# Optimization experiments

Measured on AMD Instinct MI355X. Metric: run time of the kernel, lower is better.

## Reference

```python
import jax, jax.numpy as jnp
import numpy as np

N, E, H, L, C = 65536, 524288, 256, 9, 4096
MAXID, IDD = 64, 8
INC = 3 + IDD  # geo(3) + id embedding(8)
HQ = H // 4


def setup_inputs() -> dict:
    key = jax.random.key(0)
    ks = jax.random.split(key, 18)
    s = lambda fan: 1.0 / np.sqrt(fan)
    d = {}
    d["x_geo"] = jax.random.normal(ks[0], (N, 3), jnp.float32)
    d["id_index"] = jax.random.randint(ks[1], (N,), 0, MAXID + 1)
    d["edge_index"] = jax.random.randint(ks[2], (2, E), 0, N)
    d["cluster"] = jax.random.randint(ks[3], (N,), 0, C)
    d["id_emb"] = jax.random.normal(ks[4], (MAXID + 1, IDD), jnp.float32) * 0.02
    d["enc_w1"] = jax.random.normal(ks[5], (INC, HQ), jnp.float32) * s(INC)
    d["enc_b1"] = jnp.zeros((HQ,), jnp.float32)
    d["enc_w2"] = jax.random.normal(ks[6], (HQ, HQ), jnp.float32) * s(HQ)
    d["enc_b2"] = jnp.zeros((HQ,), jnp.float32)
    d["enc_w3"] = jax.random.normal(ks[7], (HQ, H), jnp.float32) * s(HQ)
    d["enc_b3"] = jnp.zeros((H,), jnp.float32)
    d["skip_w"] = jax.random.normal(ks[8], (INC, H), jnp.float32) * s(INC)
    d["skip_b"] = jnp.zeros((H,), jnp.float32)
    d["gcn_w"] = jax.random.normal(ks[9], (L, H, H), jnp.float32) * s(H)
    d["gcn_b"] = jnp.zeros((L, H), jnp.float32)
    d["ln_g"] = jnp.ones((L, H), jnp.float32)
    d["ln_b"] = jnp.zeros((L, H), jnp.float32)
    return d


def _gelu(x):
    return jax.nn.gelu(x, approximate=False)  # torch GELU default is exact


def reference(x_geo, id_index, edge_index, cluster, id_emb,
              enc_w1, enc_b1, enc_w2, enc_b2, enc_w3, enc_b3,
              skip_w, skip_b, gcn_w, gcn_b, ln_g, ln_b):
    n = x_geo.shape[0]
    # node features: geo + id embedding
    node = jnp.concatenate([x_geo, id_emb[id_index]], axis=-1)  # [N, 11]
    # ResBottleneck encoder
    h = _gelu(node @ enc_w1 + enc_b1)
    h = _gelu(h @ enc_w2 + enc_b2)
    h = h @ enc_w3 + enc_b3
    x = _gelu(node @ skip_w + skip_b + h)  # [N, H]

    src, dst = edge_index[0], edge_index[1]
    e = src.shape[0]
    # degree with self-loops (GCN symmetric norm)
    deg = jax.ops.segment_sum(jnp.ones((e,), x.dtype), dst, num_segments=n) + 1.0
    dis = jax.lax.rsqrt(deg)  # deg^-1/2, [N]
    self_norm = (dis * dis)[:, None]
    edge_norm = (dis[src] * dis[dst])[:, None]

    orig = x
    for i in range(L):
        hi = x @ gcn_w[i]                                    # [N, H]
        msg = hi[src] * edge_norm                            # gather + scale
        agg = jax.ops.segment_sum(msg, dst, num_segments=n)  # scatter-add
        agg = agg + hi * self_norm + gcn_b[i]                # self-loop + bias
        # LayerNorm
        mu = agg.mean(-1, keepdims=True)
        var = ((agg - mu) ** 2).mean(-1, keepdims=True)
        xn = (agg - mu) * jax.lax.rsqrt(var + 1e-5) * ln_g[i] + ln_b[i]
        x = jax.nn.relu(xn)  # dropout p=1e-4 inactive in eval mode
        if i == 0:
            x = x + orig  # residual after first conv only

    # avg_pool_x: mean of node features per cluster
    cnt = jax.ops.segment_sum(jnp.ones((n,), x.dtype), cluster, num_segments=C)
    pooled = jax.ops.segment_sum(x, cluster, num_segments=C) / jnp.maximum(cnt, 1.0)[:, None]
    # F.normalize(p=2, dim=0, eps=1e-6): per-feature L2 norm across clusters
    nrm = jnp.sqrt(jnp.sum(pooled * pooled, axis=0, keepdims=True))
    return pooled / jnp.maximum(nrm, 1e-6)
```

## Files before the change

### kernel.cpp

```cpp
#include <hip/hip_runtime.h>
#include <math.h>

#define N_NODES 65536
#define N_EDGES 524288
#define HDIM 256
#define NLAYERS 9
#define NCLUST 4096
#define HQ 64
#define INCF 11

typedef __attribute__((ext_vector_type(8))) short short8v;
typedef __attribute__((ext_vector_type(4))) float f32x4;

__device__ __forceinline__ float gelu_exact(float v) {
    return 0.5f * v * (1.0f + erff(v * 0.70710678118654752440f));
}

__device__ __forceinline__ unsigned short f2bf(float f) {
    union { float f; unsigned u; } a; a.f = f;
    unsigned r = a.u + 0x7FFFu + ((a.u >> 16) & 1u);
    return (unsigned short)(r >> 16);
}

__device__ __forceinline__ float bf2f(unsigned short h) {
    union { unsigned u; float f; } a; a.u = ((unsigned)h) << 16;
    return a.f;
}

__device__ __forceinline__ void split_bf(float v, unsigned short& h, unsigned short& l) {
    h = f2bf(v);
    l = f2bf(v - bf2f(h));
}

__device__ __forceinline__ void gload16(const void* g, void* l) {
    __builtin_amdgcn_global_load_lds(
        (const __attribute__((address_space(1))) void*)g,
        (__attribute__((address_space(3))) void*)l,
        16, 0, 0);
}

__global__ __launch_bounds__(256) void encoder_kernel(
    const float* __restrict__ x_geo, const int* __restrict__ id_index,
    const float* __restrict__ id_emb,
    const float* __restrict__ w1, const float* __restrict__ b1,
    const float* __restrict__ w2, const float* __restrict__ b2,
    const float* __restrict__ w3, const float* __restrict__ b3,
    const float* __restrict__ sw, const float* __restrict__ sb,
    unsigned short* __restrict__ xh, unsigned short* __restrict__ xl)
{
    int wid = blockIdx.x * 4 + (threadIdx.x >> 6);
    int lane = threadIdx.x & 63;
    int nbase = wid * 4;
    if (nbase >= N_NODES) return;

    float nf[4][INCF];
#pragma unroll
    for (int j = 0; j < 4; ++j) {
        int node = nbase + j;
        nf[j][0] = x_geo[node * 3 + 0];
        nf[j][1] = x_geo[node * 3 + 1];
        nf[j][2] = x_geo[node * 3 + 2];
        int idv = id_index[node];
#pragma unroll
        for (int k = 0; k < 8; ++k) nf[j][3 + k] = id_emb[idv * 8 + k];
    }

    float h1[4];
    {
        float b = b1[lane];
        float a0 = b, a1 = b, a2 = b, a3 = b;
#pragma unroll
        for (int k = 0; k < INCF; ++k) {
            float wv = w1[k * HQ + lane];
            a0 += nf[0][k] * wv; a1 += nf[1][k] * wv;
            a2 += nf[2][k] * wv; a3 += nf[3][k] * wv;
        }
        h1[0] = gelu_exact(a0); h1[1] = gelu_exact(a1);
        h1[2] = gelu_exact(a2); h1[3] = gelu_exact(a3);
    }

    float h2[4];
    {
        float b = b2[lane];
        float a0 = b, a1 = b, a2 = b, a3 = b;
        for (int k = 0; k < HQ; ++k) {
            float wv = w2[k * HQ + lane];
            a0 += __shfl(h1[0], k) * wv; a1 += __shfl(h1[1], k) * wv;
            a2 += __shfl(h1[2], k) * wv; a3 += __shfl(h1[3], k) * wv;
        }
        h2[0] = gelu_exact(a0); h2[1] = gelu_exact(a1);
        h2[2] = gelu_exact(a2); h2[3] = gelu_exact(a3);
    }

    float a4[4][4];
#pragma unroll
    for (int j0 = 0; j0 < 4; ++j0) {
        float b = b3[j0 * 64 + lane] + sb[j0 * 64 + lane];
#pragma unroll
        for (int j = 0; j < 4; ++j) a4[j][j0] = b;
    }
    for (int k = 0; k < HQ; ++k) {
        float wv0 = w3[k * HDIM + 0 * 64 + lane];
        float wv1 = w3[k * HDIM + 1 * 64 + lane];
        float wv2 = w3[k * HDIM + 2 * 64 + lane];
        float wv3 = w3[k * HDIM + 3 * 64 + lane];
#pragma unroll
        for (int j = 0; j < 4; ++j) {
            float hk = __shfl(h2[j], k);
            a4[j][0] += hk * wv0; a4[j][1] += hk * wv1;
            a4[j][2] += hk * wv2; a4[j][3] += hk * wv3;
        }
    }
#pragma unroll
    for (int k = 0; k < INCF; ++k) {
        float wv0 = sw[k * HDIM + 0 * 64 + lane];
        float wv1 = sw[k * HDIM + 1 * 64 + lane];
        float wv2 = sw[k * HDIM + 2 * 64 + lane];
        float wv3 = sw[k * HDIM + 3 * 64 + lane];
#pragma unroll
        for (int j = 0; j < 4; ++j) {
            float nk = nf[j][k];
            a4[j][0] += nk * wv0; a4[j][1] += nk * wv1;
            a4[j][2] += nk * wv2; a4[j][3] += nk * wv3;
        }
    }
#pragma unroll
    for (int j = 0; j < 4; ++j) {
        int node = nbase + j;
#pragma unroll
        for (int j0 = 0; j0 < 4; ++j0) {
            float v = gelu_exact(a4[j][j0]);
            unsigned short h, l;
            split_bf(v, h, l);
            xh[(size_t)node * HDIM + j0 * 64 + lane] = h;
            xl[(size_t)node * HDIM + j0 * 64 + lane] = l;
        }
    }
}

__global__ void count_kernel(const int* __restrict__ dst, int* __restrict__ degi) {
    int e = blockIdx.x * blockDim.x + threadIdx.x;
    if (e < N_EDGES) atomicAdd(&degi[dst[e]], 1);
}

__global__ void dis_kernel(const int* __restrict__ degi, float* __restrict__ dis) {
    int n = blockIdx.x * blockDim.x + threadIdx.x;
    if (n < N_NODES) dis[n] = rsqrtf((float)degi[n] + 1.0f);
}

__global__ __launch_bounds__(1024) void scan_kernel(const int* __restrict__ degi,
                                                    int* __restrict__ off) {
    __shared__ int part[1024];
    int t = threadIdx.x;
    int base = t * 64;
    int s = 0;
    for (int j = 0; j < 64; ++j) s += degi[base + j];
    part[t] = s;
    __syncthreads();
    for (int d = 1; d < 1024; d <<= 1) {
        int v = (t >= d) ? part[t - d] : 0;
        __syncthreads();
        part[t] += v;
        __syncthreads();
    }
    int run = (t == 0) ? 0 : part[t - 1];
    for (int j = 0; j < 64; ++j) {
        off[base + j] = run;
        run += degi[base + j];
    }
    if (t == 1023) off[N_NODES] = run;
}

__global__ void fill_kernel(const int* __restrict__ src, const int* __restrict__ dst,
                            const int* __restrict__ off, int* __restrict__ cursor,
                            int* __restrict__ csr_src) {
    int e = blockIdx.x * blockDim.x + threadIdx.x;
    if (e >= N_EDGES) return;
    int d = dst[e];
    int pos = off[d] + atomicAdd(&cursor[d], 1);
    csr_src[pos] = src[e];
}

__global__ __launch_bounds__(256) void wtrans_kernel(const float* __restrict__ w,
                                                     unsigned short* __restrict__ wth,
                                                     unsigned short* __restrict__ wtl_) {
    __shared__ float t[32][257];
    int l = blockIdx.y, kb = blockIdx.x;
    const float* wl = w + (size_t)l * HDIM * HDIM + (size_t)kb * 32 * HDIM;
#pragma unroll
    for (int it = 0; it < 32; ++it) {
        int idx = it * 256 + threadIdx.x;
        t[idx >> 8][idx & 255] = wl[idx];
    }
    __syncthreads();
    unsigned short* wh = wth + (size_t)l * HDIM * HDIM + kb * 32;
    unsigned short* wl2 = wtl_ + (size_t)l * HDIM * HDIM + kb * 32;
    int k = threadIdx.x & 31, n0 = threadIdx.x >> 5;
#pragma unroll
    for (int it = 0; it < 32; ++it) {
        int n = it * 8 + n0;
        unsigned short h, lo;
        split_bf(t[k][n], h, lo);
        wh[(size_t)n * HDIM + k] = h;
        wl2[(size_t)n * HDIM + k] = lo;
    }
}

__global__ __launch_bounds__(512) void mfma_gemm_kernel(
    const unsigned short* __restrict__ Ah, const unsigned short* __restrict__ Al,
    const unsigned short* __restrict__ Bh, const unsigned short* __restrict__ Bl,
    float* __restrict__ C_)
{
    __shared__ unsigned short AsH[128 * 32];
    __shared__ unsigned short AsL[128 * 32];
    __shared__ unsigned short BsH[256 * 32];
    __shared__ unsigned short BsL[256 * 32];
    int tid = threadIdx.x;
    int w = tid >> 6, l = tid & 63;
    int bm = blockIdx.x;
    int wm = w >> 2, wn = w & 3;
    int fr = l & 15, fs = l >> 4;

    f32x4 acc[4][4];
#pragma unroll
    for (int m = 0; m < 4; ++m)
#pragma unroll
        for (int n = 0; n < 4; ++n) acc[m][n] = (f32x4){0.f, 0.f, 0.f, 0.f};

    const size_t aoff = (size_t)(bm * 128) * HDIM;
    const int rowA = tid >> 2, subA = tid & 3;
    const int sgA = subA ^ ((rowA >> 1) & 3);
    const int rowB1 = (512 + tid) >> 2;
    const int sgB1 = subA ^ ((rowB1 >> 1) & 3);

    unsigned short* lAH = &AsH[(w * 64) * 8];
    unsigned short* lAL = &AsL[(w * 64) * 8];
    unsigned short* lBH0 = &BsH[(w * 64) * 8];
    unsigned short* lBL0 = &BsL[(w * 64) * 8];
    unsigned short* lBH1 = &BsH[(512 + w * 64) * 8];
    unsigned short* lBL1 = &BsL[(512 + w * 64) * 8];

    for (int k0 = 0; k0 < HDIM; k0 += 32) {
        gload16(Ah + aoff + (size_t)rowA * HDIM + k0 + sgA * 8, lAH);
        gload16(Al + aoff + (size_t)rowA * HDIM + k0 + sgA * 8, lAL);
        gload16(Bh + (size_t)rowA * HDIM + k0 + sgA * 8, lBH0);
        gload16(Bl + (size_t)rowA * HDIM + k0 + sgA * 8, lBL0);
        gload16(Bh + (size_t)rowB1 * HDIM + k0 + sgB1 * 8, lBH1);
        gload16(Bl + (size_t)rowB1 * HDIM + k0 + sgB1 * 8, lBL1);
        asm volatile("s_waitcnt vmcnt(0)" ::: "memory");
        __syncthreads();

        short8v afh[4], afl[4], bfh[4], bfl[4];
#pragma unroll
        for (int m = 0; m < 4; ++m) {
            int row = wm * 64 + m * 16 + fr;
            int cl = row * 4 + (fs ^ ((row >> 1) & 3));
            afh[m] = *(const short8v*)&AsH[cl * 8];
            afl[m] = *(const short8v*)&AsL[cl * 8];
        }
#pragma unroll
        for (int n = 0; n < 4; ++n) {
            int row = wn * 64 + n * 16 + fr;
            int cl = row * 4 + (fs ^ ((row >> 1) & 3));
            bfh[n] = *(const short8v*)&BsH[cl * 8];
            bfl[n] = *(const short8v*)&BsL[cl * 8];
        }
#pragma unroll
        for (int m = 0; m < 4; ++m)
#pragma unroll
            for (int n = 0; n < 4; ++n) {
                acc[m][n] = __builtin_amdgcn_mfma_f32_16x16x32_bf16(
                    afh[m], bfl[n], acc[m][n], 0, 0, 0);
                acc[m][n] = __builtin_amdgcn_mfma_f32_16x16x32_bf16(
                    afl[m], bfh[n], acc[m][n], 0, 0, 0);
                acc[m][n] = __builtin_amdgcn_mfma_f32_16x16x32_bf16(
                    afh[m], bfh[n], acc[m][n], 0, 0, 0);
            }
        __syncthreads();
    }

#pragma unroll
    for (int m = 0; m < 4; ++m) {
#pragma unroll
        for (int n = 0; n < 4; ++n) {
            int col = wn * 64 + n * 16 + fr;
#pragma unroll
            for (int r = 0; r < 4; ++r) {
                int rowg = bm * 128 + wm * 64 + m * 16 + fs * 4 + r;
                C_[(size_t)rowg * HDIM + col] = acc[m][n][r];
            }
        }
    }
}

__global__ __launch_bounds__(256) void agg_ln_kernel(
    const float* __restrict__ hi, const float* __restrict__ dis,
    const int* __restrict__ off, const int* __restrict__ csr_src,
    const float* __restrict__ bias, const float* __restrict__ g,
    const float* __restrict__ bln,
    unsigned short* __restrict__ xh, unsigned short* __restrict__ xl,
    int addResidual)
{
    int gtid = blockIdx.x * blockDim.x + threadIdx.x;
    int n = gtid >> 6;
    int lane = threadIdx.x & 63;
    if (n >= N_NODES) return;
    float dn = dis[n];
    int p0 = off[n], p1 = off[n + 1];
    int deg = p1 - p0;
    float4 vself = *(const float4*)(hi + (size_t)n * HDIM + lane * 4);
    float4 bv = *(const float4*)(bias + lane * 4);
    float4 gv = *(const float4*)(g + lane * 4);
    float4 bb = *(const float4*)(bln + lane * 4);

    float4 acc = make_float4(0.f, 0.f, 0.f, 0.f);
    float4 v0, v1, v2, v3;
    float wt0 = 0.f, wt1 = 0.f, wt2 = 0.f, wt3 = 0.f;
    if (deg > 0) { int s = csr_src[p0 + 0]; wt0 = dis[s]; v0 = *(const float4*)(hi + (size_t)s * HDIM + lane * 4); }
    if (deg > 1) { int s = csr_src[p0 + 1]; wt1 = dis[s]; v1 = *(const float4*)(hi + (size_t)s * HDIM + lane * 4); }
    if (deg > 2) { int s = csr_src[p0 + 2]; wt2 = dis[s]; v2 = *(const float4*)(hi + (size_t)s * HDIM + lane * 4); }
    if (deg > 3) { int s = csr_src[p0 + 3]; wt3 = dis[s]; v3 = *(const float4*)(hi + (size_t)s * HDIM + lane * 4); }
    int pp = 0;
    for (; pp + 4 <= deg; pp += 4) {
        float4 v = v0; float wv = wt0 * dn;
        if (pp + 4 < deg) { int s = csr_src[p0 + pp + 4]; wt0 = dis[s]; v0 = *(const float4*)(hi + (size_t)s * HDIM + lane * 4); }
        acc.x += v.x * wv; acc.y += v.y * wv; acc.z += v.z * wv; acc.w += v.w * wv;
        v = v1; wv = wt1 * dn;
        if (pp + 5 < deg) { int s = csr_src[p0 + pp + 5]; wt1 = dis[s]; v1 = *(const float4*)(hi + (size_t)s * HDIM + lane * 4); }
        acc.x += v.x * wv; acc.y += v.y * wv; acc.z += v.z * wv; acc.w += v.w * wv;
        v = v2; wv = wt2 * dn;
        if (pp + 6 < deg) { int s = csr_src[p0 + pp + 6]; wt2 = dis[s]; v2 = *(const float4*)(hi + (size_t)s * HDIM + lane * 4); }
        acc.x += v.x * wv; acc.y += v.y * wv; acc.z += v.z * wv; acc.w += v.w * wv;
        v = v3; wv = wt3 * dn;
        if (pp + 7 < deg) { int s = csr_src[p0 + pp + 7]; wt3 = dis[s]; v3 = *(const float4*)(hi + (size_t)s * HDIM + lane * 4); }
        acc.x += v.x * wv; acc.y += v.y * wv; acc.z += v.z * wv; acc.w += v.w * wv;
    }
    int r = deg - pp;
    if (r > 0) { float wv = wt0 * dn; acc.x += v0.x * wv; acc.y += v0.y * wv; acc.z += v0.z * wv; acc.w += v0.w * wv; }
    if (r > 1) { float wv = wt1 * dn; acc.x += v1.x * wv; acc.y += v1.y * wv; acc.z += v1.z * wv; acc.w += v1.w * wv; }
    if (r > 2) { float wv = wt2 * dn; acc.x += v2.x * wv; acc.y += v2.y * wv; acc.z += v2.z * wv; acc.w += v2.w * wv; }

    {
        float wv = dn * dn;
        acc.x += vself.x * wv + bv.x;
        acc.y += vself.y * wv + bv.y;
        acc.z += vself.z * wv + bv.z;
        acc.w += vself.w * wv + bv.w;
    }
    float s1 = acc.x + acc.y + acc.z + acc.w;
    float s2 = acc.x * acc.x + acc.y * acc.y + acc.z * acc.z + acc.w * acc.w;
#pragma unroll
    for (int m = 1; m < 64; m <<= 1) {
        s1 += __shfl_xor(s1, m);
        s2 += __shfl_xor(s2, m);
    }
    float mu = s1 * (1.0f / 256.0f);
    float var = s2 * (1.0f / 256.0f) - mu * mu;
    float inv = rsqrtf(var + 1e-5f);
    float4 res;
    res.x = fmaxf((acc.x - mu) * inv * gv.x + bb.x, 0.0f);
    res.y = fmaxf((acc.y - mu) * inv * gv.y + bb.y, 0.0f);
    res.z = fmaxf((acc.z - mu) * inv * gv.z + bb.z, 0.0f);
    res.w = fmaxf((acc.w - mu) * inv * gv.w + bb.w, 0.0f);
    if (addResidual) {
        ushort4 oh = *(const ushort4*)(xh + (size_t)n * HDIM + lane * 4);
        ushort4 ol = *(const ushort4*)(xl + (size_t)n * HDIM + lane * 4);
        res.x += bf2f(oh.x) + bf2f(ol.x);
        res.y += bf2f(oh.y) + bf2f(ol.y);
        res.z += bf2f(oh.z) + bf2f(ol.z);
        res.w += bf2f(oh.w) + bf2f(ol.w);
    }
    ushort4 h4, l4;
    split_bf(res.x, h4.x, l4.x);
    split_bf(res.y, h4.y, l4.y);
    split_bf(res.z, h4.z, l4.z);
    split_bf(res.w, h4.w, l4.w);
    *(ushort4*)(xh + (size_t)n * HDIM + lane * 4) = h4;
    *(ushort4*)(xl + (size_t)n * HDIM + lane * 4) = l4;
}

__global__ void ccount_kernel(const int* __restrict__ cluster, int* __restrict__ ccnt) {
    int n = blockIdx.x * blockDim.x + threadIdx.x;
    if (n < N_NODES) atomicAdd(&ccnt[cluster[n]], 1);
}

__global__ __launch_bounds__(1024) void cscan_kernel(const int* __restrict__ ccnt,
                                                     int* __restrict__ coff) {
    __shared__ int part[1024];
    int t = threadIdx.x;
    int s = 0;
    for (int j = 0; j < 4; ++j) s += ccnt[t * 4 + j];
    part[t] = s;
    __syncthreads();
    for (int d = 1; d < 1024; d <<= 1) {
        int v = (t >= d) ? part[t - d] : 0;
        __syncthreads();
        part[t] += v;
        __syncthreads();
    }
    int run = (t == 0) ? 0 : part[t - 1];
    for (int j = 0; j < 4; ++j) {
        coff[t * 4 + j] = run;
        run += ccnt[t * 4 + j];
    }
    if (t == 1023) coff[NCLUST] = run;
}

__global__ void cfill_kernel(const int* __restrict__ cluster, const int* __restrict__ coff,
                             int* __restrict__ ccur, int* __restrict__ cnodes) {
    int n = blockIdx.x * blockDim.x + threadIdx.x;
    if (n >= N_NODES) return;
    int c = cluster[n];
    cnodes[coff[c] + atomicAdd(&ccur[c], 1)] = n;
}

__global__ __launch_bounds__(256) void pool_csr_kernel(const unsigned short* __restrict__ xh,
                                                       const unsigned short* __restrict__ xl,
                                                       const int* __restrict__ coff,
                                                       const int* __restrict__ cnodes,
                                                       float* __restrict__ pooled) {
    int gtid = blockIdx.x * blockDim.x + threadIdx.x;
    int c = gtid >> 6;
    int lane = threadIdx.x & 63;
    if (c >= NCLUST) return;
    int p0 = coff[c], p1 = coff[c + 1];
    float4 acc = make_float4(0.f, 0.f, 0.f, 0.f);
    for (int p = p0; p < p1; ++p) {
        int n = cnodes[p];
        ushort4 h4 = *(const ushort4*)(xh + (size_t)n * HDIM + lane * 4);
        ushort4 l4 = *(const ushort4*)(xl + (size_t)n * HDIM + lane * 4);
        acc.x += bf2f(h4.x) + bf2f(l4.x);
        acc.y += bf2f(h4.y) + bf2f(l4.y);
        acc.z += bf2f(h4.z) + bf2f(l4.z);
        acc.w += bf2f(h4.w) + bf2f(l4.w);
    }
    float inv = 1.0f / fmaxf((float)(p1 - p0), 1.0f);
    acc.x *= inv; acc.y *= inv; acc.z *= inv; acc.w *= inv;
    *(float4*)(pooled + (size_t)c * HDIM + lane * 4) = acc;
}

__global__ __launch_bounds__(256) void colsq_kernel(const float* __restrict__ pooled,
                                                    float* __restrict__ colsq) {
    int h = threadIdx.x;
    int c0 = blockIdx.x * 16;
    float sq = 0.f;
    for (int cc = 0; cc < 16; ++cc) {
        float v = pooled[(size_t)(c0 + cc) * HDIM + h];
        sq += v * v;
    }
    atomicAdd(&colsq[h], sq);
}

__global__ __launch_bounds__(256) void final_kernel(const float* __restrict__ pooled,
                                                    const float* __restrict__ colsq,
                                                    float* __restrict__ out) {
    int i = blockIdx.x * blockDim.x + threadIdx.x;
    if (i >= NCLUST * HDIM) return;
    int h = i & (HDIM - 1);
    float nrm = fmaxf(sqrtf(colsq[h]), 1e-6f);
    out[i] = pooled[i] / nrm;
}

extern "C" void kernel_launch(void* const* d_in, const int* in_sizes, int n_in,
                              void* d_out, int out_size, void* d_ws, size_t ws_size,
                              hipStream_t stream) {
    const float* x_geo   = (const float*)d_in[0];
    const int*   id_index = (const int*)d_in[1];
    const int*   edge_index = (const int*)d_in[2];
    const int*   cluster = (const int*)d_in[3];
    const float* id_emb  = (const float*)d_in[4];
    const float* enc_w1  = (const float*)d_in[5];
    const float* enc_b1  = (const float*)d_in[6];
    const float* enc_w2  = (const float*)d_in[7];
    const float* enc_b2  = (const float*)d_in[8];
    const float* enc_w3  = (const float*)d_in[9];
    const float* enc_b3  = (const float*)d_in[10];
    const float* skip_w  = (const float*)d_in[11];
    const float* skip_b  = (const float*)d_in[12];
    const float* gcn_w   = (const float*)d_in[13];
    const float* gcn_b   = (const float*)d_in[14];
    const float* ln_g    = (const float*)d_in[15];
    const float* ln_b    = (const float*)d_in[16];
    float* out = (float*)d_out;

    char* ws = (char*)d_ws;
    size_t o = 0;
    auto alloc = [&](size_t bytes) {
        char* p = ws + o;
        o += (bytes + 255) & ~(size_t)255;
        return p;
    };
    float*          hi     = (float*)alloc((size_t)N_NODES * HDIM * 4);
    unsigned short* xh     = (unsigned short*)alloc((size_t)N_NODES * HDIM * 2);
    unsigned short* xl     = (unsigned short*)alloc((size_t)N_NODES * HDIM * 2);
    unsigned short* wth    = (unsigned short*)alloc((size_t)NLAYERS * HDIM * HDIM * 2);
    unsigned short* wtl    = (unsigned short*)alloc((size_t)NLAYERS * HDIM * HDIM * 2);
    int*   degi    = (int*)alloc((size_t)N_NODES * 4);
    float* dis     = (float*)alloc((size_t)N_NODES * 4);
    int*   off     = (int*)alloc((size_t)(N_NODES + 1) * 4);
    int*   cursor  = (int*)alloc((size_t)N_NODES * 4);
    int*   csr_src = (int*)alloc((size_t)N_EDGES * 4);
    int*   ccnt    = (int*)alloc((size_t)NCLUST * 4);
    int*   coff    = (int*)alloc((size_t)(NCLUST + 1) * 4);
    int*   ccur    = (int*)alloc((size_t)NCLUST * 4);
    int*   cnodes  = (int*)alloc((size_t)N_NODES * 4);
    float* pooled  = (float*)alloc((size_t)NCLUST * HDIM * 4);
    float* colsq   = (float*)alloc((size_t)256 * 4);

    const int* esrc = edge_index;
    const int* edst = edge_index + N_EDGES;

    hipMemsetAsync(degi, 0, (size_t)N_NODES * 4, stream);
    hipMemsetAsync(cursor, 0, (size_t)N_NODES * 4, stream);
    hipMemsetAsync(ccnt, 0, (size_t)NCLUST * 4, stream);
    hipMemsetAsync(ccur, 0, (size_t)NCLUST * 4, stream);
    hipMemsetAsync(colsq, 0, (size_t)256 * 4, stream);

    encoder_kernel<<<N_NODES / 16, 256, 0, stream>>>(
        x_geo, id_index, id_emb, enc_w1, enc_b1, enc_w2, enc_b2, enc_w3, enc_b3,
        skip_w, skip_b, xh, xl);

    wtrans_kernel<<<dim3(8, NLAYERS), 256, 0, stream>>>(gcn_w, wth, wtl);

    count_kernel<<<N_EDGES / 256, 256, 0, stream>>>(edst, degi);
    dis_kernel<<<N_NODES / 256, 256, 0, stream>>>(degi, dis);
    scan_kernel<<<1, 1024, 0, stream>>>(degi, off);
    fill_kernel<<<N_EDGES / 256, 256, 0, stream>>>(esrc, edst, off, cursor, csr_src);

    ccount_kernel<<<N_NODES / 256, 256, 0, stream>>>(cluster, ccnt);
    cscan_kernel<<<1, 1024, 0, stream>>>(ccnt, coff);
    cfill_kernel<<<N_NODES / 256, 256, 0, stream>>>(cluster, coff, ccur, cnodes);

    for (int i = 0; i < NLAYERS; ++i) {
        mfma_gemm_kernel<<<N_NODES / 128, 512, 0, stream>>>(
            xh, xl, wth + (size_t)i * HDIM * HDIM, wtl + (size_t)i * HDIM * HDIM, hi);
        agg_ln_kernel<<<N_NODES / 4, 256, 0, stream>>>(
            hi, dis, off, csr_src, gcn_b + (size_t)i * HDIM,
            ln_g + (size_t)i * HDIM, ln_b + (size_t)i * HDIM, xh, xl, (i == 0) ? 1 : 0);
    }

    pool_csr_kernel<<<NCLUST / 4, 256, 0, stream>>>(xh, xl, coff, cnodes, pooled);
    colsq_kernel<<<NCLUST / 16, 256, 0, stream>>>(pooled, colsq);
    final_kernel<<<NCLUST * HDIM / 256, 256, 0, stream>>>(pooled, colsq, out);
}
```

Measured before the change: 1.522 ms.

## Double-buffer LDS tiles in MFMA GEMM to overlap global loads with compute

```diff
diff --git a/kernel.cpp b/kernel.cpp
--- a/kernel.cpp
+++ b/kernel.cpp
@@ -211,10 +211,10 @@
     const unsigned short* __restrict__ Bh, const unsigned short* __restrict__ Bl,
     float* __restrict__ C_)
 {
-    __shared__ unsigned short AsH[128 * 32];
-    __shared__ unsigned short AsL[128 * 32];
-    __shared__ unsigned short BsH[256 * 32];
-    __shared__ unsigned short BsL[256 * 32];
+    __shared__ unsigned short AsH[2][128 * 32];
+    __shared__ unsigned short AsL[2][128 * 32];
+    __shared__ unsigned short BsH[2][256 * 32];
+    __shared__ unsigned short BsL[2][256 * 32];
     int tid = threadIdx.x;
     int w = tid >> 6, l = tid & 63;
     int bm = blockIdx.x;
@@ -232,22 +232,27 @@
     const int sgA = subA ^ ((rowA >> 1) & 3);
     const int rowB1 = (512 + tid) >> 2;
     const int sgB1 = subA ^ ((rowB1 >> 1) & 3);
-
-    unsigned short* lAH = &AsH[(w * 64) * 8];
-    unsigned short* lAL = &AsL[(w * 64) * 8];
-    unsigned short* lBH0 = &BsH[(w * 64) * 8];
-    unsigned short* lBL0 = &BsL[(w * 64) * 8];
-    unsigned short* lBH1 = &BsH[(512 + w * 64) * 8];
-    unsigned short* lBL1 = &BsL[(512 + w * 64) * 8];
-
-    for (int k0 = 0; k0 < HDIM; k0 += 32) {
-        gload16(Ah + aoff + (size_t)rowA * HDIM + k0 + sgA * 8, lAH);
-        gload16(Al + aoff + (size_t)rowA * HDIM + k0 + sgA * 8, lAL);
-        gload16(Bh + (size_t)rowA * HDIM + k0 + sgA * 8, lBH0);
-        gload16(Bl + (size_t)rowA * HDIM + k0 + sgA * 8, lBL0);
-        gload16(Bh + (size_t)rowB1 * HDIM + k0 + sgB1 * 8, lBH1);
-        gload16(Bl + (size_t)rowB1 * HDIM + k0 + sgB1 * 8, lBL1);
-        asm volatile("s_waitcnt vmcnt(0)" ::: "memory");
+    const int ldsOff = (w * 64) * 8;
+
+    auto STAGE = [&](int b, int k0) {
+        gload16(Ah + aoff + (size_t)rowA * HDIM + k0 + sgA * 8, &AsH[b][ldsOff]);
+        gload16(Al + aoff + (size_t)rowA * HDIM + k0 + sgA * 8, &AsL[b][ldsOff]);
+        gload16(Bh + (size_t)rowA * HDIM + k0 + sgA * 8, &BsH[b][ldsOff]);
+        gload16(Bl + (size_t)rowA * HDIM + k0 + sgA * 8, &BsL[b][ldsOff]);
+        gload16(Bh + (size_t)rowB1 * HDIM + k0 + sgB1 * 8, &BsH[b][4096 + ldsOff]);
+        gload16(Bl + (size_t)rowB1 * HDIM + k0 + sgB1 * 8, &BsL[b][4096 + ldsOff]);
+    };
+
+    STAGE(0, 0);
+#pragma unroll
+    for (int t = 0; t < 8; ++t) {
+        const int cur = t & 1;
+        if (t < 7) {
+            STAGE(cur ^ 1, (t + 1) * 32);
+            asm volatile("s_waitcnt vmcnt(6)" ::: "memory");
+        } else {
+            asm volatile("s_waitcnt vmcnt(0)" ::: "memory");
+        }
         __syncthreads();
 
         short8v afh[4], afl[4], bfh[4], bfl[4];
@@ -255,15 +260,15 @@
         for (int m = 0; m < 4; ++m) {
             int row = wm * 64 + m * 16 + fr;
             int cl = row * 4 + (fs ^ ((row >> 1) & 3));
-            afh[m] = *(const short8v*)&AsH[cl * 8];
-            afl[m] = *(const short8v*)&AsL[cl * 8];
+            afh[m] = *(const short8v*)&AsH[cur][cl * 8];
+            afl[m] = *(const short8v*)&AsL[cur][cl * 8];
         }
 #pragma unroll
         for (int n = 0; n < 4; ++n) {
             int row = wn * 64 + n * 16 + fr;
             int cl = row * 4 + (fs ^ ((row >> 1) & 3));
-            bfh[n] = *(const short8v*)&BsH[cl * 8];
-            bfl[n] = *(const short8v*)&BsL[cl * 8];
+            bfh[n] = *(const short8v*)&BsH[cur][cl * 8];
+            bfl[n] = *(const short8v*)&BsL[cur][cl * 8];
         }
 #pragma unroll
         for (int m = 0; m < 4; ++m)
```

New measurement: 1.515 ms. About the same (-0.5%).
